# Kernel optimization log

Measured on AMD Instinct MI355X. Metric: run time of the kernel, lower is better.

Reference implementation:

```python
import jax, jax.numpy as jnp
import numpy as np

# Constants matching the module's forward-time configuration
NUM_STAGES = 2
HIDDEN_LENGTH = (512, 1024)   # per-stage video token lengths; S = sum = 1536
ENC_LEN = 128                 # text/encoder token length per sample
B, H, D = 8, 16, 64           # batch (interleaved over stages), heads, head_dim
SEQLENS = (np.array([640, 480, 560, 400], np.int32),     # valid lens, stage 0 (Lc=640)
           np.array([1152, 864, 1008, 720], np.int32))   # valid lens, stage 1 (Lc=1152)


def _pack_indices(seqlens, lc):
    return np.concatenate([i * lc + np.arange(l) for i, l in enumerate(seqlens)]).astype(np.int32)


def setup_inputs() -> dict:
    key = jax.random.key(0)
    ks = jax.random.split(key, 6)
    S = sum(HIDDEN_LENGTH)
    inp = {
        'query':         jax.random.normal(ks[0], (B, S, H, D), jnp.float32),
        'key':           jax.random.normal(ks[1], (B, S, H, D), jnp.float32),
        'value':         jax.random.normal(ks[2], (B, S, H, D), jnp.float32),
        'encoder_query': jax.random.normal(ks[3], (B, ENC_LEN, H, D), jnp.float32),
        'encoder_key':   jax.random.normal(ks[4], (B, ENC_LEN, H, D), jnp.float32),
        'encoder_value': jax.random.normal(ks[5], (B, ENC_LEN, H, D), jnp.float32),
        'indices_0': jnp.asarray(_pack_indices(SEQLENS[0], ENC_LEN + HIDDEN_LENGTH[0])),
        'indices_1': jnp.asarray(_pack_indices(SEQLENS[1], ENC_LEN + HIDDEN_LENGTH[1])),
        'seqlens_0': jnp.asarray(SEQLENS[0]),
        'seqlens_1': jnp.asarray(SEQLENS[1]),
        'heads': 16,
        'scale': jnp.asarray(0.125, jnp.float32),  # 1/sqrt(D)
    }
    return inp


def reference(query, key, value, encoder_query, encoder_key, encoder_value,
              indices_0, indices_1, seqlens_0, seqlens_1, heads, scale):
    # Per stage: take the interleaved batch slice, prepend encoder tokens,
    # run non-causal varlen attention (padded + key-masked == flash_attn_varlen),
    # then gather the valid (packed) rows — faithful to index_first_axis packing.
    indices = (indices_0, indices_1)
    seqlens = (seqlens_0, seqlens_1)
    neg = jnp.finfo(query.dtype).min
    outs = []
    i_sum = 0
    for idx, L in enumerate(HIDDEN_LENGTH):
        q_s = jnp.concatenate([encoder_query[idx::NUM_STAGES], query[idx::NUM_STAGES, i_sum:i_sum + L]], axis=1)
        k_s = jnp.concatenate([encoder_key[idx::NUM_STAGES],   key[idx::NUM_STAGES,   i_sum:i_sum + L]], axis=1)
        v_s = jnp.concatenate([encoder_value[idx::NUM_STAGES], value[idx::NUM_STAGES, i_sum:i_sum + L]], axis=1)
        lc = q_s.shape[1]                                    # enc_len + L
        kmask = jnp.arange(lc)[None, :] < seqlens[idx][:, None]   # [b, lc] key validity
        scores = jnp.einsum('bqhd,bkhd->bhqk', q_s, k_s) * scale  # [b,h,lc,lc]
        scores = jnp.where(kmask[:, None, None, :], scores, neg)
        attn = jax.nn.softmax(scores, axis=-1)
        o = jnp.einsum('bhqk,bkhd->bqhd', attn, v_s)              # [b,lc,h,d]
        o_flat = o.reshape(-1, o.shape[2], o.shape[3])            # [(b*lc),h,d]
        outs.append(o_flat[indices[idx]])                          # pack valid rows
        i_sum += L
    return jnp.concatenate(outs, axis=0)  # [total_packed_tokens, H, D]
```

## Files before the change

### kernel.cpp

```cpp
#include <hip/hip_runtime.h>
#include <hip/hip_bf16.h>

typedef __attribute__((ext_vector_type(8))) __bf16 bf16x8;
typedef __attribute__((ext_vector_type(8))) short short8;
typedef __attribute__((ext_vector_type(4))) float f32x4;
typedef __attribute__((ext_vector_type(4))) unsigned int uint4v;

#define KS 72
#define LOG2E 1.44269504088896340736f

__device__ __forceinline__ unsigned pack2bf(float lo, float hi) {
    unsigned a = __builtin_bit_cast(unsigned, lo) + 0x8000u;
    unsigned b = __builtin_bit_cast(unsigned, hi) + 0x8000u;
    return __builtin_amdgcn_perm(b, a, 0x07060302u);
}

__device__ __forceinline__ bf16x8 ldfrag(const short* p) {
    short8 s = *reinterpret_cast<const short8*>(p);
    return __builtin_bit_cast(bf16x8, s);
}

__global__ __launch_bounds__(256, 6) void vfa_kernel(
    const float* __restrict__ qv, const float* __restrict__ kv, const float* __restrict__ vv,
    const float* __restrict__ eq, const float* __restrict__ ek, const float* __restrict__ ev,
    const float* __restrict__ scale_p, float* __restrict__ out)
{
    constexpr int H = 16, Dh = 64, ENC = 128, SV = 1536;
    constexpr int SS_CUM[9] = {0,288,544,768,960,1120,1264,1392,1504};
    constexpr int SEQL[8] = {1152,1008,864,720,640,560,480,400};
    constexpr int QTN[8]  = {18,16,14,12,10,9,8,7};
    constexpr int OB[8]   = {2080,4096,3232,5104,0,1120,640,1680};
    constexpr int BB[8]   = {1,5,3,7,0,4,2,6};
    constexpr int ISUM[8] = {512,512,512,512,0,0,0,0};

    __shared__ __align__(16) short smem[2*64*KS];
    short* kbuf = smem;
    short* vbuf = smem + 64*KS;

    const int bid = blockIdx.x;
    int ss = 0;
    #pragma unroll
    for (int i = 1; i < 8; ++i) ss += (bid >= SS_CUM[i]) ? 1 : 0;
    const int seqlen   = SEQL[ss];
    const int nqt      = QTN[ss];
    const int b        = BB[ss];
    const int isum     = ISUM[ss];
    const int out_base = OB[ss];
    const int local    = bid - SS_CUM[ss];
    const int head     = local / nqt;
    const int qt       = local - head * nqt;

    const int tid  = threadIdx.x;
    const int wave = tid >> 6;
    const int lane = tid & 63;
    const int quad = lane >> 4;
    const int l15  = lane & 15;

    const float qmul = scale_p[0] * LOG2E;

    const int qrow = qt*64 + wave*16 + l15;
    const float* qrp;
    if (qrow < ENC) qrp = eq + ((b*ENC + qrow)*H + head)*Dh;
    else            qrp = qv + (((b*SV + isum) + (qrow - ENC))*H + head)*Dh;
    bf16x8 qfrag[2];
    #pragma unroll
    for (int f = 0; f < 2; ++f) {
        const float* p = qrp + f*32 + quad*8;
        float4 a = *reinterpret_cast<const float4*>(p);
        float4 c = *reinterpret_cast<const float4*>(p + 4);
        uint4v u;
        u[0] = pack2bf(a.x*qmul, a.y*qmul);
        u[1] = pack2bf(a.z*qmul, a.w*qmul);
        u[2] = pack2bf(c.x*qmul, c.y*qmul);
        u[3] = pack2bf(c.z*qmul, c.w*qmul);
        qfrag[f] = __builtin_bit_cast(bf16x8, u);
    }

    f32x4 acc[4];
    #pragma unroll
    for (int dt = 0; dt < 4; ++dt) acc[dt] = {0.f,0.f,0.f,0.f};
    float m_s = -INFINITY, l_s = 0.f;

    const int key_local = tid >> 2;
    const int dbase     = (tid & 3) * 16;
    const int nkt = (seqlen + 63) >> 6;
    const int src_base = l15 + ((quad & 1) << 5);

    for (int kt = 0; kt < nkt; ++kt) {
        if (kt) __syncthreads();
        {
            const int kr = kt*64 + key_local;
            const float *krow, *vrow;
            if (kr < ENC) {
                krow = ek + ((b*ENC + kr)*H + head)*Dh;
                vrow = ev + ((b*ENC + kr)*H + head)*Dh;
            } else {
                const int row = (b*SV + isum) + (kr - ENC);
                krow = kv + (row*H + head)*Dh;
                vrow = vv + (row*H + head)*Dh;
            }
            float4 kf[4], vf[4];
            #pragma unroll
            for (int j = 0; j < 4; ++j) {
                kf[j] = *reinterpret_cast<const float4*>(krow + dbase + 4*j);
                vf[j] = *reinterpret_cast<const float4*>(vrow + dbase + 4*j);
            }
            uint4v kp;
            kp[0] = pack2bf(kf[0].x, kf[0].y);
            kp[1] = pack2bf(kf[0].z, kf[0].w);
            kp[2] = pack2bf(kf[1].x, kf[1].y);
            kp[3] = pack2bf(kf[1].z, kf[1].w);
            *reinterpret_cast<uint4v*>(&kbuf[key_local*KS + dbase]) = kp;
            kp[0] = pack2bf(kf[2].x, kf[2].y);
            kp[1] = pack2bf(kf[2].z, kf[2].w);
            kp[2] = pack2bf(kf[3].x, kf[3].y);
            kp[3] = pack2bf(kf[3].z, kf[3].w);
            *reinterpret_cast<uint4v*>(&kbuf[key_local*KS + dbase + 8]) = kp;
            #pragma unroll
            for (int j = 0; j < 4; ++j) {
                float e[4] = {vf[j].x, vf[j].y, vf[j].z, vf[j].w};
                #pragma unroll
                for (int i = 0; i < 4; ++i) {
                    unsigned u = __builtin_bit_cast(unsigned, e[i]) + 0x8000u;
                    vbuf[(dbase + 4*j + i)*KS + key_local] = (short)(u >> 16);
                }
            }
        }
        __syncthreads();

        const int rem  = seqlen - kt*64;
        const int nsub = (rem >= 64) ? 4 : (rem >> 4);

        float s[4][4];
        #pragma unroll
        for (int sub = 0; sub < 4; ++sub) {
            if (sub < nsub) {
                const short* kr0 = &kbuf[(sub*16 + l15)*KS + quad*8];
                f32x4 sv = {0.f,0.f,0.f,0.f};
                sv = __builtin_amdgcn_mfma_f32_16x16x32_bf16(ldfrag(kr0),      qfrag[0], sv, 0,0,0);
                sv = __builtin_amdgcn_mfma_f32_16x16x32_bf16(ldfrag(kr0 + 32), qfrag[1], sv, 0,0,0);
                #pragma unroll
                for (int r = 0; r < 4; ++r) s[sub][r] = sv[r];
            } else {
                #pragma unroll
                for (int r = 0; r < 4; ++r) s[sub][r] = -INFINITY;
            }
        }

        float mx = s[0][0];
        #pragma unroll
        for (int sub = 0; sub < 4; ++sub)
            #pragma unroll
            for (int r = 0; r < 4; ++r) mx = fmaxf(mx, s[sub][r]);
        mx = fmaxf(mx, __shfl_xor(mx, 16, 64));
        mx = fmaxf(mx, __shfl_xor(mx, 32, 64));
        const float mn = fmaxf(m_s, mx);
        const float alpha = __builtin_amdgcn_exp2f(m_s - mn);
        m_s = mn;
        #pragma unroll
        for (int dt = 0; dt < 4; ++dt)
            #pragma unroll
            for (int r = 0; r < 4; ++r) acc[dt][r] *= alpha;

        float rs = 0.f;
        unsigned pk[4][2];
        #pragma unroll
        for (int sub = 0; sub < 4; ++sub) {
            float p0 = __builtin_amdgcn_exp2f(s[sub][0] - mn);
            float p1 = __builtin_amdgcn_exp2f(s[sub][1] - mn);
            float p2 = __builtin_amdgcn_exp2f(s[sub][2] - mn);
            float p3 = __builtin_amdgcn_exp2f(s[sub][3] - mn);
            rs += (p0 + p1) + (p2 + p3);
            pk[sub][0] = pack2bf(p0, p1);
            pk[sub][1] = pack2bf(p2, p3);
        }
        rs += __shfl_xor(rs, 16, 64);
        rs += __shfl_xor(rs, 32, 64);
        l_s = l_s * alpha + rs;

        #pragma unroll
        for (int kstep = 0; kstep < 2; ++kstep) {
            if (kstep == 0 || nsub > 2) {
                uint4v pf;
                #pragma unroll
                for (int p = 0; p < 4; ++p) {
                    const int sl = src_base + ((p >> 1) << 4);
                    int va = __shfl((int)pk[kstep*2 + 0][p & 1], sl, 64);
                    int vb = __shfl((int)pk[kstep*2 + 1][p & 1], sl, 64);
                    pf[p] = (quad & 2) ? (unsigned)vb : (unsigned)va;
                }
                bf16x8 pfr = __builtin_bit_cast(bf16x8, pf);
                #pragma unroll
                for (int dt = 0; dt < 4; ++dt) {
                    bf16x8 vfr = ldfrag(&vbuf[(dt*16 + l15)*KS + kstep*32 + quad*8]);
                    acc[dt] = __builtin_amdgcn_mfma_f32_16x16x32_bf16(vfr, pfr, acc[dt], 0,0,0);
                }
            }
        }
    }

    __syncthreads();
    float* tbuf = reinterpret_cast<float*>(smem);
    const float inv = 1.0f / l_s;
    #pragma unroll
    for (int dt = 0; dt < 4; ++dt)
        #pragma unroll
        for (int r = 0; r < 4; ++r)
            tbuf[(wave*16 + l15)*68 + dt*16 + quad*4 + r] = acc[dt][r] * inv;
    __syncthreads();

    const int rowl = tid >> 2;
    const int grow = qt*64 + rowl;
    if (grow < seqlen) {
        float* orow = out + (size_t)(out_base + grow)*(H*Dh) + head*Dh;
        const float* trow = tbuf + rowl*68 + (tid & 3)*4;
        #pragma unroll
        for (int c = 0; c < 4; ++c)
            *reinterpret_cast<float4*>(orow + (tid & 3)*4 + c*16) =
                *reinterpret_cast<const float4*>(trow + c*16);
    }
}

extern "C" void kernel_launch(void* const* d_in, const int* in_sizes, int n_in,
                              void* d_out, int out_size, void* d_ws, size_t ws_size,
                              hipStream_t stream) {
    const float* q     = (const float*)d_in[0];
    const float* k     = (const float*)d_in[1];
    const float* v     = (const float*)d_in[2];
    const float* eq    = (const float*)d_in[3];
    const float* ek    = (const float*)d_in[4];
    const float* ev    = (const float*)d_in[5];
    const float* scale = (const float*)d_in[11];
    float* out = (float*)d_out;

    vfa_kernel<<<dim3(1504), dim3(256), 0, stream>>>(q, k, v, eq, ek, ev, scale, out);
}
```

Baseline: 218.5 us.

## Use 128-row query tiles with 8 waves sharing each K/V tile

Doubles the block to 512 threads so each block handles 128 query rows and every K/V tile staged in shared memory is reused by twice as many waves, halving global K/V loads and conversion work per query row. The staging is split so half the threads convert K and the other half convert V with a transposed layout, writing V as packed 8-byte stores instead of scalar shorts. The output epilogue becomes two passes through the shared buffer. In exchange, the grid halves to 768 blocks, which can leave compute units less evenly loaded. The larger blocks with a higher launch-bound target also put more pressure on registers.

After: 210.9 us. -3.5%, faster.

```diff
diff --git a/kernel.cpp b/kernel.cpp
--- a/kernel.cpp
+++ b/kernel.cpp
@@ -5,6 +5,7 @@
 typedef __attribute__((ext_vector_type(8))) short short8;
 typedef __attribute__((ext_vector_type(4))) float f32x4;
 typedef __attribute__((ext_vector_type(4))) unsigned int uint4v;
+typedef __attribute__((ext_vector_type(2))) unsigned int uint2v;
 
 #define KS 72
 #define LOG2E 1.44269504088896340736f
@@ -20,15 +21,15 @@
     return __builtin_bit_cast(bf16x8, s);
 }
 
-__global__ __launch_bounds__(256, 6) void vfa_kernel(
+__global__ __launch_bounds__(512, 8) void vfa_kernel(
     const float* __restrict__ qv, const float* __restrict__ kv, const float* __restrict__ vv,
     const float* __restrict__ eq, const float* __restrict__ ek, const float* __restrict__ ev,
     const float* __restrict__ scale_p, float* __restrict__ out)
 {
     constexpr int H = 16, Dh = 64, ENC = 128, SV = 1536;
-    constexpr int SS_CUM[9] = {0,288,544,768,960,1120,1264,1392,1504};
+    constexpr int SS_CUM[9] = {0,144,272,384,480,560,640,704,768};
     constexpr int SEQL[8] = {1152,1008,864,720,640,560,480,400};
-    constexpr int QTN[8]  = {18,16,14,12,10,9,8,7};
+    constexpr int QTN[8]  = {9,8,7,6,5,5,4,4};
     constexpr int OB[8]   = {2080,4096,3232,5104,0,1120,640,1680};
     constexpr int BB[8]   = {1,5,3,7,0,4,2,6};
     constexpr int ISUM[8] = {512,512,512,512,0,0,0,0};
@@ -58,7 +59,7 @@
 
     const float qmul = scale_p[0] * LOG2E;
 
-    const int qrow = qt*64 + wave*16 + l15;
+    const int qrow = qt*128 + wave*16 + l15;
     const float* qrp;
     if (qrow < ENC) qrp = eq + ((b*ENC + qrow)*H + head)*Dh;
     else            qrp = qv + (((b*SV + isum) + (qrow - ENC))*H + head)*Dh;
@@ -66,13 +67,13 @@
     #pragma unroll
     for (int f = 0; f < 2; ++f) {
         const float* p = qrp + f*32 + quad*8;
-        float4 a = *reinterpret_cast<const float4*>(p);
-        float4 c = *reinterpret_cast<const float4*>(p + 4);
+        f32x4 a = *reinterpret_cast<const f32x4*>(p);
+        f32x4 c = *reinterpret_cast<const f32x4*>(p + 4);
         uint4v u;
-        u[0] = pack2bf(a.x*qmul, a.y*qmul);
-        u[1] = pack2bf(a.z*qmul, a.w*qmul);
-        u[2] = pack2bf(c.x*qmul, c.y*qmul);
-        u[3] = pack2bf(c.z*qmul, c.w*qmul);
+        u[0] = pack2bf(a[0]*qmul, a[1]*qmul);
+        u[1] = pack2bf(a[2]*qmul, a[3]*qmul);
+        u[2] = pack2bf(c[0]*qmul, c[1]*qmul);
+        u[3] = pack2bf(c[2]*qmul, c[3]*qmul);
         qfrag[f] = __builtin_bit_cast(bf16x8, u);
     }
 
@@ -81,49 +82,53 @@
     for (int dt = 0; dt < 4; ++dt) acc[dt] = {0.f,0.f,0.f,0.f};
     float m_s = -INFINITY, l_s = 0.f;
 
-    const int key_local = tid >> 2;
-    const int dbase     = (tid & 3) * 16;
+    const int t2  = tid & 255;
+    const int klk = t2 >> 2;
+    const int kd  = (t2 & 3) * 16;
+    const int vk0 = (t2 & 15) * 4;
+    const int vd0 = (t2 >> 4) * 4;
+
     const int nkt = (seqlen + 63) >> 6;
     const int src_base = l15 + ((quad & 1) << 5);
 
     for (int kt = 0; kt < nkt; ++kt) {
         if (kt) __syncthreads();
-        {
-            const int kr = kt*64 + key_local;
-            const float *krow, *vrow;
-            if (kr < ENC) {
-                krow = ek + ((b*ENC + kr)*H + head)*Dh;
-                vrow = ev + ((b*ENC + kr)*H + head)*Dh;
-            } else {
-                const int row = (b*SV + isum) + (kr - ENC);
-                krow = kv + (row*H + head)*Dh;
-                vrow = vv + (row*H + head)*Dh;
-            }
-            float4 kf[4], vf[4];
+        if (tid < 256) {
+            const int kr = kt*64 + klk;
+            const float* krow;
+            if (kr < ENC) krow = ek + ((b*ENC + kr)*H + head)*Dh;
+            else          krow = kv + (((b*SV + isum) + (kr - ENC))*H + head)*Dh;
+            f32x4 kf0 = *reinterpret_cast<const f32x4*>(krow + kd);
+            f32x4 kf1 = *reinterpret_cast<const f32x4*>(krow + kd + 4);
+            f32x4 kf2 = *reinterpret_cast<const f32x4*>(krow + kd + 8);
+            f32x4 kf3 = *reinterpret_cast<const f32x4*>(krow + kd + 12);
+            uint4v kp;
+            kp[0] = pack2bf(kf0[0], kf0[1]);
+            kp[1] = pack2bf(kf0[2], kf0[3]);
+            kp[2] = pack2bf(kf1[0], kf1[1]);
+            kp[3] = pack2bf(kf1[2], kf1[3]);
+            *reinterpret_cast<uint4v*>(&kbuf[klk*KS + kd]) = kp;
+            kp[0] = pack2bf(kf2[0], kf2[1]);
+            kp[1] = pack2bf(kf2[2], kf2[3]);
+            kp[2] = pack2bf(kf3[0], kf3[1]);
+            kp[3] = pack2bf(kf3[2], kf3[3]);
+            *reinterpret_cast<uint4v*>(&kbuf[klk*KS + kd + 8]) = kp;
+        } else {
+            f32x4 vf[4];
+            #pragma unroll
+            for (int i = 0; i < 4; ++i) {
+                const int kr = kt*64 + vk0 + i;
+                const float* vrow;
+                if (kr < ENC) vrow = ev + ((b*ENC + kr)*H + head)*Dh;
+                else          vrow = vv + (((b*SV + isum) + (kr - ENC))*H + head)*Dh;
+                vf[i] = *reinterpret_cast<const f32x4*>(vrow + vd0);
+            }
             #pragma unroll
             for (int j = 0; j < 4; ++j) {
-                kf[j] = *reinterpret_cast<const float4*>(krow + dbase + 4*j);
-                vf[j] = *reinterpret_cast<const float4*>(vrow + dbase + 4*j);
-            }
-            uint4v kp;
-            kp[0] = pack2bf(kf[0].x, kf[0].y);
-            kp[1] = pack2bf(kf[0].z, kf[0].w);
-            kp[2] = pack2bf(kf[1].x, kf[1].y);
-            kp[3] = pack2bf(kf[1].z, kf[1].w);
-            *reinterpret_cast<uint4v*>(&kbuf[key_local*KS + dbase]) = kp;
-            kp[0] = pack2bf(kf[2].x, kf[2].y);
-            kp[1] = pack2bf(kf[2].z, kf[2].w);
-            kp[2] = pack2bf(kf[3].x, kf[3].y);
-            kp[3] = pack2bf(kf[3].z, kf[3].w);
-            *reinterpret_cast<uint4v*>(&kbuf[key_local*KS + dbase + 8]) = kp;
-            #pragma unroll
-            for (int j = 0; j < 4; ++j) {
-                float e[4] = {vf[j].x, vf[j].y, vf[j].z, vf[j].w};
-                #pragma unroll
-                for (int i = 0; i < 4; ++i) {
-                    unsigned u = __builtin_bit_cast(unsigned, e[i]) + 0x8000u;
-                    vbuf[(dbase + 4*j + i)*KS + key_local] = (short)(u >> 16);
-                }
+                uint2v w;
+                w[0] = pack2bf(vf[0][j], vf[1][j]);
+                w[1] = pack2bf(vf[2][j], vf[3][j]);
+                *reinterpret_cast<uint2v*>(&vbuf[(vd0 + j)*KS + vk0]) = w;
             }
         }
         __syncthreads();
@@ -202,22 +207,26 @@
     __syncthreads();
     float* tbuf = reinterpret_cast<float*>(smem);
     const float inv = 1.0f / l_s;
-    #pragma unroll
-    for (int dt = 0; dt < 4; ++dt)
-        #pragma unroll
-        for (int r = 0; r < 4; ++r)
-            tbuf[(wave*16 + l15)*68 + dt*16 + quad*4 + r] = acc[dt][r] * inv;
-    __syncthreads();
-
-    const int rowl = tid >> 2;
-    const int grow = qt*64 + rowl;
-    if (grow < seqlen) {
-        float* orow = out + (size_t)(out_base + grow)*(H*Dh) + head*Dh;
-        const float* trow = tbuf + rowl*68 + (tid & 3)*4;
-        #pragma unroll
-        for (int c = 0; c < 4; ++c)
-            *reinterpret_cast<float4*>(orow + (tid & 3)*4 + c*16) =
-                *reinterpret_cast<const float4*>(trow + c*16);
+    const int rowl = tid >> 3;
+    const int colb = (tid & 7) * 8;
+    #pragma unroll
+    for (int p = 0; p < 2; ++p) {
+        if (p) __syncthreads();
+        if ((wave >> 2) == p) {
+            #pragma unroll
+            for (int dt = 0; dt < 4; ++dt) {
+                f32x4 t = acc[dt] * inv;
+                *reinterpret_cast<f32x4*>(&tbuf[((wave & 3)*16 + l15)*68 + dt*16 + quad*4]) = t;
+            }
+        }
+        __syncthreads();
+        const int grow = qt*128 + p*64 + rowl;
+        if (grow < seqlen) {
+            float* orow = out + (size_t)(out_base + grow)*(H*Dh) + head*Dh + colb;
+            const float* trow = tbuf + rowl*68 + colb;
+            *reinterpret_cast<float4*>(orow)     = *reinterpret_cast<const float4*>(trow);
+            *reinterpret_cast<float4*>(orow + 4) = *reinterpret_cast<const float4*>(trow + 4);
+        }
     }
 }
 
@@ -233,5 +242,5 @@
     const float* scale = (const float*)d_in[11];
     float* out = (float*)d_out;
 
-    vfa_kernel<<<dim3(1504), dim3(256), 0, stream>>>(q, k, v, eq, ek, ev, scale, out);
-}
+    vfa_kernel<<<dim3(768), dim3(512), 0, stream>>>(q, k, v, eq, ek, ev, scale, out);
+}
```
